# Performance work log

Measured on AMD Instinct MI355X. Metric: run time of the kernel, lower is better.

## Reference

```python
import jax, jax.numpy as jnp
import numpy as np

N_HEAD = 16
NEG_INF = -1e30  # finite mask value, safe for softmax/grad


def setup_inputs() -> dict:
    key = jax.random.key(0)
    k1, k2, k3 = jax.random.split(key, 3)
    B, T, C = 4, 2049, 1024
    x = jax.random.normal(k1, (B, T, C), dtype=jnp.float32)
    W_attn = jax.random.normal(k2, (C, 3 * C), dtype=jnp.float32) * (1.0 / np.sqrt(C))
    W_proj = jax.random.normal(k3, (C, C), dtype=jnp.float32) * (1.0 / np.sqrt(C))
    return {"x": x, "W_attn": W_attn, "W_proj": W_proj}


def reference(x, W_attn, W_proj):
    B, T, C = x.shape
    H = N_HEAD
    D = C // H
    qkv = x @ W_attn                                  # (B, T, 3C)
    q, k, v = jnp.split(qkv, 3, axis=-1)
    q = q.reshape(B, T, H, D).transpose(0, 2, 1, 3)   # (B, H, T, D)
    k = k.reshape(B, T, H, D).transpose(0, 2, 1, 3)
    v = v.reshape(B, T, H, D).transpose(0, 2, 1, 3)
    # hybrid mask: causal tril, but state token (row 0) attends to ALL positions
    mask = jnp.tril(jnp.ones((T, T), dtype=bool))
    mask = mask.at[0, :].set(True)
    scale = 1.0 / np.sqrt(D)
    scores = jnp.einsum('bhtd,bhsd->bhts', q, k) * scale
    scores = jnp.where(mask[None, None, :, :], scores, NEG_INF)
    att = jax.nn.softmax(scores, axis=-1)
    y = jnp.einsum('bhts,bhsd->bhtd', att, v)         # (B, H, T, D)
    y = y.transpose(0, 2, 1, 3).reshape(B, T, C)
    return y @ W_proj
```

## Files before the change

### kernel.cpp

```cpp
#include <hip/hip_runtime.h>

typedef __attribute__((ext_vector_type(8))) __bf16 bf16x8;
typedef __attribute__((ext_vector_type(4))) __bf16 bf16x4;
typedef __attribute__((ext_vector_type(4))) float f32x4;

#define GLDS(g, l) __builtin_amdgcn_global_load_lds( \
    (__attribute__((address_space(1))) void*)(void*)(g), \
    (__attribute__((address_space(3))) void*)(void*)(l), 16, 0, 0)

constexpr int T_REAL = 2049;
constexpr int Tp     = 2112;
constexpr int Mreal  = 8196;
constexpr int Mp     = 8448;
constexpr int GK     = 1024;

constexpr float QSCALE = 0.125f * 1.4426950408889634f;

__global__ __launch_bounds__(256) void cvt_x(const float* __restrict__ x,
                                             __bf16* __restrict__ xb) {
    size_t i = ((size_t)blockIdx.x * 256 + threadIdx.x) * 4;
    float4 v = make_float4(0.f, 0.f, 0.f, 0.f);
    if (i < (size_t)Mreal * GK) v = *(const float4*)(x + i);
    bf16x4 o;
    o.x = (__bf16)v.x; o.y = (__bf16)v.y; o.z = (__bf16)v.z; o.w = (__bf16)v.w;
    *(bf16x4*)(xb + i) = o;
}

__global__ __launch_bounds__(256) void transpose_w(const float* __restrict__ W,
                                                   __bf16* __restrict__ Wt,
                                                   int K, int N) {
    __shared__ float tile[64][65];
    const int n0 = blockIdx.x * 64, k0 = blockIdx.y * 64;
    const int tx = threadIdx.x & 63, ty = threadIdx.x >> 6;
#pragma unroll
    for (int j = 0; j < 16; j++) {
        int rk = ty + j * 4;
        tile[rk][tx] = W[(size_t)(k0 + rk) * N + n0 + tx];
    }
    __syncthreads();
#pragma unroll
    for (int j = 0; j < 16; j++) {
        int rn = ty + j * 4;
        Wt[(size_t)(n0 + rn) * K + k0 + tx] = (__bf16)tile[tx][rn];
    }
}

__global__ __launch_bounds__(256) void transpose_v(const __bf16* __restrict__ v,
                                                   __bf16* __restrict__ vT) {
    __shared__ __bf16 tl[64][72];
    const int bh = blockIdx.y, t0 = blockIdx.x * 64;
    const int tid = threadIdx.x;
    const __bf16* src = v + ((size_t)bh * Tp + t0) * 64;
    {
        const int r = tid >> 3, c = (tid & 7) * 8;
        *(bf16x8*)&tl[r][c]      = *(const bf16x8*)(src + r * 64 + c);
        *(bf16x8*)&tl[r + 32][c] = *(const bf16x8*)(src + (r + 32) * 64 + c);
    }
    __syncthreads();
    __bf16* dst = vT + (size_t)bh * 64 * Tp + t0;
    {
        const int d = tid >> 3, tc = (tid & 7) * 8;
        bf16x8 a, b;
#pragma unroll
        for (int i = 0; i < 8; i++) {
            a[i] = tl[tc + i][d];
            b[i] = tl[tc + i][d + 32];
        }
        *(bf16x8*)(dst + (size_t)d * Tp + tc)        = a;
        *(bf16x8*)(dst + (size_t)(d + 32) * Tp + tc) = b;
    }
}

__global__ __launch_bounds__(512)
void gemm256(const __bf16* __restrict__ A, const __bf16* __restrict__ Bt,
             __bf16* __restrict__ qout, __bf16* __restrict__ kout,
             __bf16* __restrict__ vout) {
    __shared__ __align__(16) __bf16 As[2][16384];
    __shared__ __align__(16) __bf16 Bs[2][16384];

    const int tid = threadIdx.x, lane = tid & 63, w = tid >> 6;
    const int wr = w >> 2, wc = w & 3;
    const int quad = lane >> 4, l15 = lane & 15, l7 = l15 & 7;
    const int m0 = blockIdx.y * 256, n0 = blockIdx.x * 256;

    const int sr = tid >> 3;
    const int sc = ((tid & 7) ^ (sr & 7)) * 8;
    const __bf16* ag = A  + (size_t)(m0 + sr) * GK + sc;
    const __bf16* bg = Bt + (size_t)(n0 + sr) * GK + sc;
    const int ldst = tid * 8;

#define STG_A(T, h) do { const __bf16* s_ = ag + (size_t)(h) * 128 * GK + (T) * 64; \
    GLDS(s_, &As[(T) & 1][(h) * 8192 + ldst]); \
    GLDS(s_ + (size_t)64 * GK, &As[(T) & 1][(h) * 8192 + 4096 + ldst]); } while (0)
#define STG_B(T, h) do { const __bf16* s_ = bg + (size_t)(h) * 128 * GK + (T) * 64; \
    GLDS(s_, &Bs[(T) & 1][(h) * 8192 + ldst]); \
    GLDS(s_ + (size_t)64 * GK, &Bs[(T) & 1][(h) * 8192 + 4096 + ldst]); } while (0)

    f32x4 acc[8][4] = {};
    bf16x8 a[8], b0[4], b1[4];

    STG_A(0, 0); STG_B(0, 1); STG_A(0, 1); STG_B(0, 0); STG_A(1, 0); STG_B(1, 1);
    asm volatile("s_waitcnt vmcnt(4)" ::: "memory");
    __builtin_amdgcn_s_barrier();

    constexpr int NT = GK / 64;

#pragma unroll 1
    for (int T = 0; T < NT; ++T) {
        const int p = T & 1;

#pragma unroll
        for (int f = 0; f < 4; ++f) {
            const int R = f * 32 + wr * 16 + l15;
            a[f * 2 + 0] = *(const bf16x8*)&As[p][R * 64 + ((quad ^ l7) * 8)];
            a[f * 2 + 1] = *(const bf16x8*)&As[p][R * 64 + (((4 + quad) ^ l7) * 8)];
        }
#pragma unroll
        for (int n = 0; n < 2; ++n) {
            const int R = n * 64 + wc * 16 + l15;
            b0[n * 2 + 0] = *(const bf16x8*)&Bs[p][R * 64 + ((quad ^ l7) * 8)];
            b0[n * 2 + 1] = *(const bf16x8*)&Bs[p][R * 64 + (((4 + quad) ^ l7) * 8)];
        }
        if (T + 1 < NT) { STG_A(T + 1, 1); STG_B(T + 1, 0); }
        __builtin_amdgcn_s_barrier();
        asm volatile("s_waitcnt lgkmcnt(0)" ::: "memory");
        __builtin_amdgcn_sched_barrier(0);
        __builtin_amdgcn_s_setprio(1);
#pragma unroll
        for (int f = 0; f < 4; ++f)
#pragma unroll
            for (int n = 0; n < 2; ++n) {
                acc[f][n] = __builtin_amdgcn_mfma_f32_16x16x32_bf16(a[f*2+0], b0[n*2+0], acc[f][n], 0, 0, 0);
                acc[f][n] = __builtin_amdgcn_mfma_f32_16x16x32_bf16(a[f*2+1], b0[n*2+1], acc[f][n], 0, 0, 0);
            }
        __builtin_amdgcn_s_setprio(0);
        __builtin_amdgcn_s_barrier();

#pragma unroll
        for (int n = 0; n < 2; ++n) {
            const int R = 128 + n * 64 + wc * 16 + l15;
            b1[n * 2 + 0] = *(const bf16x8*)&Bs[p][R * 64 + ((quad ^ l7) * 8)];
            b1[n * 2 + 1] = *(const bf16x8*)&Bs[p][R * 64 + (((4 + quad) ^ l7) * 8)];
        }
        __builtin_amdgcn_s_barrier();
        asm volatile("s_waitcnt lgkmcnt(0)" ::: "memory");
        __builtin_amdgcn_sched_barrier(0);
        __builtin_amdgcn_s_setprio(1);
#pragma unroll
        for (int f = 0; f < 4; ++f)
#pragma unroll
            for (int n = 0; n < 2; ++n) {
                acc[f][2+n] = __builtin_amdgcn_mfma_f32_16x16x32_bf16(a[f*2+0], b1[n*2+0], acc[f][2+n], 0, 0, 0);
                acc[f][2+n] = __builtin_amdgcn_mfma_f32_16x16x32_bf16(a[f*2+1], b1[n*2+1], acc[f][2+n], 0, 0, 0);
            }
        __builtin_amdgcn_s_setprio(0);
        __builtin_amdgcn_s_barrier();

#pragma unroll
        for (int f = 0; f < 4; ++f) {
            const int R = 128 + f * 32 + wr * 16 + l15;
            a[f * 2 + 0] = *(const bf16x8*)&As[p][R * 64 + ((quad ^ l7) * 8)];
            a[f * 2 + 1] = *(const bf16x8*)&As[p][R * 64 + (((4 + quad) ^ l7) * 8)];
        }
        if (T + 2 < NT) STG_A(T + 2, 0);
        __builtin_amdgcn_s_barrier();
        asm volatile("s_waitcnt lgkmcnt(0)" ::: "memory");
        __builtin_amdgcn_sched_barrier(0);
        __builtin_amdgcn_s_setprio(1);
#pragma unroll
        for (int f = 0; f < 4; ++f)
#pragma unroll
            for (int n = 0; n < 2; ++n) {
                acc[4+f][2+n] = __builtin_amdgcn_mfma_f32_16x16x32_bf16(a[f*2+0], b1[n*2+0], acc[4+f][2+n], 0, 0, 0);
                acc[4+f][2+n] = __builtin_amdgcn_mfma_f32_16x16x32_bf16(a[f*2+1], b1[n*2+1], acc[4+f][2+n], 0, 0, 0);
            }
        __builtin_amdgcn_s_setprio(0);
        __builtin_amdgcn_s_barrier();

        if (T + 2 < NT) STG_B(T + 2, 1);
        __builtin_amdgcn_s_barrier();
        asm volatile("s_waitcnt lgkmcnt(0)" ::: "memory");
        __builtin_amdgcn_sched_barrier(0);
        __builtin_amdgcn_s_setprio(1);
#pragma unroll
        for (int f = 0; f < 4; ++f)
#pragma unroll
            for (int n = 0; n < 2; ++n) {
                acc[4+f][n] = __builtin_amdgcn_mfma_f32_16x16x32_bf16(a[f*2+0], b0[n*2+0], acc[4+f][n], 0, 0, 0);
                acc[4+f][n] = __builtin_amdgcn_mfma_f32_16x16x32_bf16(a[f*2+1], b0[n*2+1], acc[4+f][n], 0, 0, 0);
            }
        __builtin_amdgcn_s_setprio(0);
        if (T < NT - 2) { asm volatile("s_waitcnt vmcnt(4)" ::: "memory"); }
        else            { asm volatile("s_waitcnt vmcnt(0)" ::: "memory"); }
        __builtin_amdgcn_s_barrier();
    }
#undef STG_A
#undef STG_B

    const int which = n0 >> 10;
    __bf16* op = (which == 0) ? qout : (which == 1) ? kout : vout;
    const float scl = (which == 0) ? QSCALE : 1.0f;
    __bf16* ep = &As[0][0];
    const int rr = tid >> 4, cc = tid & 15;
#pragma unroll
    for (int f = 0; f < 8; ++f) {
        __syncthreads();
#pragma unroll
        for (int n = 0; n < 4; ++n) {
            const int col = (n & 1) * 64 + wc * 16 + (n >> 1) * 128 + l15;
#pragma unroll
            for (int r = 0; r < 4; ++r)
                ep[(wr * 16 + quad * 4 + r) * 264 + col] = (__bf16)(acc[f][n][r] * scl);
        }
        __syncthreads();
        const int m = m0 + (f & 3) * 32 + (f >> 2) * 128 + rr;
        if (m < Mreal) {
            const int b = m / T_REAL;
            const int t = m - b * T_REAL;
#pragma unroll
            for (int g = 0; g < 2; ++g) {
                const int c8 = (cc + g * 16) * 8;
                bf16x8 vv = *(const bf16x8*)&ep[rr * 264 + c8];
                const int gc = n0 + c8;
                const int h = (gc >> 6) & 15;
                *(bf16x8*)&op[((size_t)(b * 16 + h) * Tp + t) * 64 + (gc & 63)] = vv;
            }
        }
    }
}

template <int EPI>
__global__ __launch_bounds__(256)
void gemm128(const __bf16* __restrict__ A, const __bf16* __restrict__ Bt,
             float* __restrict__ outp,
             __bf16* __restrict__ qout, __bf16* __restrict__ kout,
             __bf16* __restrict__ vout) {
    __shared__ __bf16 As[128 * 64];
    __shared__ __bf16 Bs[128 * 64];

    const int tid = threadIdx.x, lane = tid & 63, w = tid >> 6;
    const int wr = w >> 1, wc = w & 1;
    const int quad = lane >> 4, l15 = lane & 15, l7 = l15 & 7;
    const int m0 = blockIdx.y * 128, n0 = blockIdx.x * 128;

    const int row0 = w * 32 + (lane >> 3);
    const int gc8 = ((lane & 7) ^ ((lane >> 3) & 7)) * 8;
    const __bf16* agp = A + (size_t)(m0 + row0) * GK + gc8;
    const __bf16* bgp = Bt + (size_t)(n0 + row0) * GK + gc8;
    __bf16* lap = &As[(w * 256 + lane) * 8];
    __bf16* lbp = &Bs[(w * 256 + lane) * 8];

    f32x4 acc[4][4] = {};

    for (int k0 = 0; k0 < GK; k0 += 64) {
#pragma unroll
        for (int s = 0; s < 4; s++) {
            GLDS(agp + (size_t)s * 8 * GK + k0, lap + s * 512);
            GLDS(bgp + (size_t)s * 8 * GK + k0, lbp + s * 512);
        }
        __syncthreads();
#pragma unroll
        for (int kk = 0; kk < 2; kk++) {
            bf16x8 fa[4], fb[4];
#pragma unroll
            for (int i = 0; i < 4; i++)
                fa[i] = *(const bf16x8*)&As[(wr * 64 + i * 16 + l15) * 64 + (((kk * 4 + quad) ^ l7) * 8)];
#pragma unroll
            for (int j = 0; j < 4; j++)
                fb[j] = *(const bf16x8*)&Bs[(wc * 64 + j * 16 + l15) * 64 + (((kk * 4 + quad) ^ l7) * 8)];
#pragma unroll
            for (int i = 0; i < 4; i++)
#pragma unroll
                for (int j = 0; j < 4; j++)
                    acc[i][j] = __builtin_amdgcn_mfma_f32_16x16x32_bf16(fa[i], fb[j], acc[i][j], 0, 0, 0);
        }
        __syncthreads();
    }

    if constexpr (EPI == 0) {
        const int which = n0 >> 10;
        const int h = ((n0 + wc * 64) >> 6) & 15;
        __bf16* op = (which == 0) ? qout : (which == 1) ? kout : vout;
        const float scl = (which == 0) ? QSCALE : 1.0f;
        __bf16* wls = &As[w * 2048];
#pragma unroll
        for (int p = 0; p < 2; p++) {
            if (p) __syncthreads();
#pragma unroll
            for (int i2 = 0; i2 < 2; i2++)
#pragma unroll
                for (int j = 0; j < 4; j++)
#pragma unroll
                    for (int r = 0; r < 4; r++) {
                        const int lrow = i2 * 16 + quad * 4 + r;
                        const int cX = (j * 2 + (l15 >> 3)) ^ (lrow & 7);
                        wls[lrow * 64 + cX * 8 + (l15 & 7)] =
                            (__bf16)(acc[p * 2 + i2][j][r] * scl);
                    }
            __syncthreads();
#pragma unroll
            for (int it = 0; it < 4; it++) {
                const int lrow = (lane >> 3) + it * 8;
                bf16x8 vv = *(const bf16x8*)&wls[lrow * 64 + (((lane & 7) ^ (lrow & 7)) * 8)];
                const int m = m0 + wr * 64 + p * 32 + lrow;
                if (m < Mreal) {
                    const int b = m / T_REAL;
                    const int t = m - b * T_REAL;
                    *(bf16x8*)&op[(((size_t)(b * 16 + h)) * Tp + t) * 64 + (lane & 7) * 8] = vv;
                }
            }
        }
    } else {
        float* wlf = (float*)&As[0] + w * 1024;
#pragma unroll
        for (int p = 0; p < 4; p++) {
            if (p) __syncthreads();
#pragma unroll
            for (int j = 0; j < 4; j++)
#pragma unroll
                for (int r = 0; r < 4; r++) {
                    const int lrow = quad * 4 + r;
                    const int cX = (j * 4 + (l15 >> 2)) ^ (lrow & 7);
                    wlf[lrow * 64 + cX * 4 + (l15 & 3)] = acc[p][j][r];
                }
            __syncthreads();
#pragma unroll
            for (int it = 0; it < 4; it++) {
                const int lrow = lane >> 2;
                const int c = (lane & 3) + it * 4;
                f32x4 vv = *(const f32x4*)&wlf[lrow * 64 + ((c ^ (lrow & 7)) * 4)];
                const int m = m0 + wr * 64 + p * 16 + lrow;
                if (m < Mreal)
                    *(f32x4*)&outp[(size_t)m * 1024 + n0 + wc * 64 + c * 4] = vv;
            }
        }
    }
}

__global__ __launch_bounds__(512, 8)
void attn(const __bf16* __restrict__ q, const __bf16* __restrict__ kk,
          const __bf16* __restrict__ vT, __bf16* __restrict__ y) {
    __shared__ __bf16 Ks[2][64 * 64];
    __shared__ __bf16 Vs[2][64 * 64];
    __shared__ __bf16 Pq[8][16 * 32];

    static const int QA[17] = {0,31,29,27,25,23,21,19,17,15,13,11,9,7,5,3,1};
    static const int QB[17] = {32,30,28,26,24,22,20,18,16,14,12,10,8,6,4,2,-1};

    const int tid = threadIdx.x, lane = tid & 63, w = tid >> 6;
    const int quad = lane >> 4, l15 = lane & 15;
    const int l7 = l15 & 7;
    const int z = blockIdx.x;
    const int slot = z >> 6;
    const int zz = z & 63;
    const int bh = (zz & 7) * 8 + (zz >> 3);

    const int qtA = QA[slot];
    const int qt = (w < 4) ? qtA : QB[slot];
    const bool active = qt >= 0;
    const int qts = active ? qt : 0;
    const int q0 = qts * 64;
    const int qg = q0 + (w & 3) * 16 + l15;
    const int myNt = (qts == 0) ? 32 : qts;
    const int ntmaxB = (qtA == 0) ? 32 : qtA;

    const __bf16* kgb = kk + (size_t)bh * Tp * 64;
    const __bf16* vgb = vT + (size_t)bh * 64 * Tp;
    const int b = bh >> 4, h = bh & 15;

    const int r0 = tid >> 3;
    const int s0 = ((tid & 7) ^ (r0 & 7)) * 8;
    const int koff = r0 * 64 + s0;
    const int voff = r0 * Tp + s0;

    const int pswz = (((l15 >> 1) & 3) << 1) ^ ((l15 >> 3) << 2);

    bf16x8 qa0, qa1;
    {
        const __bf16* qp = q + ((size_t)bh * Tp + qg) * 64 + quad * 8;
        qa0 = *(const bf16x8*)qp;
        qa1 = *(const bf16x8*)(qp + 32);
    }

    f32x4 o[4] = {};
    float mrow = -3e38f, lrow = 0.f;

    GLDS(kgb + koff, &Ks[0][tid * 8]);
    GLDS(vgb + voff, &Vs[0][tid * 8]);

    int cur = 0;
    for (int nt = 0; nt <= ntmaxB; ++nt) {
        __syncthreads();
        if (nt < ntmaxB) {
            GLDS(kgb + (size_t)(nt + 1) * 4096 + koff, &Ks[cur ^ 1][tid * 8]);
            GLDS(vgb + (size_t)(nt + 1) * 64 + voff, &Vs[cur ^ 1][tid * 8]);
        }
        if (active && nt <= myNt) {
            const int kv0 = nt * 64;

            f32x4 st[4];
#pragma unroll
            for (int j = 0; j < 4; j++) {
                const __bf16* krow = &Ks[cur][(j * 16 + l15) * 64];
                bf16x8 klo = *(const bf16x8*)(krow + ((quad ^ l7) * 8));
                bf16x8 khi = *(const bf16x8*)(krow + (((quad + 4) ^ l7) * 8));
                f32x4 zzv = {0.f, 0.f, 0.f, 0.f};
                zzv = __builtin_amdgcn_mfma_f32_16x16x32_bf16(klo, qa0, zzv, 0, 0, 0);
                st[j] = __builtin_amdgcn_mfma_f32_16x16x32_bf16(khi, qa1, zzv, 0, 0, 0);
            }

            if (nt >= qts) {
#pragma unroll
                for (int j = 0; j < 4; j++)
#pragma unroll
                    for (int r = 0; r < 4; r++) {
                        const int kvg = kv0 + j * 16 + quad * 4 + r;
                        const bool valid = (kvg <= qg) || (qg == 0 && kvg < T_REAL);
                        st[j][r] = valid ? st[j][r] : -1e30f;
                    }
            }

            float mx = -3e38f;
#pragma unroll
            for (int j = 0; j < 4; j++)
#pragma unroll
                for (int r = 0; r < 4; r++) mx = fmaxf(mx, st[j][r]);
            mx = fmaxf(mx, __shfl_xor(mx, 16));
            mx = fmaxf(mx, __shfl_xor(mx, 32));
            if (!__all(mx - mrow <= 8.0f)) {
                const float mn = fmaxf(mrow, mx);
                const float alpha = __builtin_amdgcn_exp2f(mrow - mn);
                mrow = mn;
                lrow *= alpha;
#pragma unroll
                for (int nf = 0; nf < 4; nf++)
#pragma unroll
                    for (int r = 0; r < 4; r++) o[nf][r] *= alpha;
            }

            float rs = 0.f;
            bf16x4 pk[4];
#pragma unroll
            for (int j = 0; j < 4; j++) {
                float p0 = __builtin_amdgcn_exp2f(st[j][0] - mrow);
                float p1 = __builtin_amdgcn_exp2f(st[j][1] - mrow);
                float p2 = __builtin_amdgcn_exp2f(st[j][2] - mrow);
                float p3 = __builtin_amdgcn_exp2f(st[j][3] - mrow);
                rs += (p0 + p1) + (p2 + p3);
                pk[j].x = (__bf16)p0; pk[j].y = (__bf16)p1;
                pk[j].z = (__bf16)p2; pk[j].w = (__bf16)p3;
            }
            rs += __shfl_xor(rs, 16);
            rs += __shfl_xor(rs, 32);
            lrow += rs;

#pragma unroll
            for (int h2 = 0; h2 < 2; ++h2) {
                *(bf16x4*)&Pq[w][l15 * 32 + (((0 + quad) ^ pswz) * 4)] = pk[2 * h2];
                *(bf16x4*)&Pq[w][l15 * 32 + (((4 + quad) ^ pswz) * 4)] = pk[2 * h2 + 1];
                bf16x8 pb = *(const bf16x8*)&Pq[w][l15 * 32 + (((quad * 2) ^ pswz) * 4)];
#pragma unroll
                for (int nf = 0; nf < 4; nf++) {
                    bf16x8 va = *(const bf16x8*)&Vs[cur][(nf * 16 + l15) * 64 + (((h2 * 4 + quad) ^ l7) * 8)];
                    o[nf] = __builtin_amdgcn_mfma_f32_16x16x32_bf16(va, pb, o[nf], 0, 0, 0);
                }
            }
        }
        cur ^= 1;
    }

    if (active && qg < T_REAL) {
        const float inv = 1.0f / lrow;
        __bf16* yp = y + ((size_t)(b * T_REAL + qg)) * 1024 + h * 64 + quad * 4;
#pragma unroll
        for (int nf = 0; nf < 4; nf++) {
            bf16x4 pko;
            pko.x = (__bf16)(o[nf][0] * inv);
            pko.y = (__bf16)(o[nf][1] * inv);
            pko.z = (__bf16)(o[nf][2] * inv);
            pko.w = (__bf16)(o[nf][3] * inv);
            *(bf16x4*)(yp + nf * 16) = pko;
        }
    }
}

extern "C" void kernel_launch(void* const* d_in, const int* in_sizes, int n_in,
                              void* d_out, int out_size, void* d_ws, size_t ws_size,
                              hipStream_t stream) {
    const float* x  = (const float*)d_in[0];
    const float* Wa = (const float*)d_in[1];
    const float* Wp = (const float*)d_in[2];
    float* out = (float*)d_out;

    char* ws = (char*)d_ws;
    constexpr size_t SZ_XB  = (size_t)Mp * GK * 2;
    constexpr size_t SZ_WAT = (size_t)3072 * GK * 2;
    constexpr size_t SZ_WPT = (size_t)1024 * GK * 2;
    constexpr size_t SZ_QK  = (size_t)64 * Tp * 64 * 2;
    __bf16* xb   = (__bf16*)(ws);
    __bf16* WaT  = (__bf16*)(ws + SZ_XB);
    __bf16* WpT  = (__bf16*)(ws + SZ_XB + SZ_WAT);
    __bf16* qb   = (__bf16*)(ws + SZ_XB + SZ_WAT + SZ_WPT);
    __bf16* kb   = (__bf16*)(ws + SZ_XB + SZ_WAT + SZ_WPT + SZ_QK);
    __bf16* vTb  = (__bf16*)(ws + SZ_XB + SZ_WAT + SZ_WPT + 2 * SZ_QK);
    __bf16* shrd = (__bf16*)(ws + SZ_XB + SZ_WAT + SZ_WPT + 3 * SZ_QK);
    __bf16* vpre = shrd;
    __bf16* yb   = shrd;

    cvt_x<<<(Mp * GK) / 1024, 256, 0, stream>>>(x, xb);
    transpose_w<<<dim3(48, 16), 256, 0, stream>>>(Wa, WaT, 1024, 3072);
    transpose_w<<<dim3(16, 16), 256, 0, stream>>>(Wp, WpT, 1024, 1024);

    gemm256<<<dim3(12, 33), 512, 0, stream>>>(xb, WaT, qb, kb, vpre);
    transpose_v<<<dim3(33, 64), 256, 0, stream>>>(vpre, vTb);
    attn<<<1088, 512, 0, stream>>>(qb, kb, vTb, yb);
    gemm128<1><<<dim3(8, 65), 256, 0, stream>>>(yb, WpT, out, nullptr, nullptr, nullptr);
}
```

Baseline: 291.2 us.

## Switch attention to 32x32x16 MFMA with register-only P via permlane32 swap

Rewrites the attention inner loop to use 32x32x16 bf16 MFMA, with each wave owning 32 query rows and blocks shrunk to 256 threads. The P matrix is packed with v_cvt_pk_bf16_f32 and rearranged across lanes with v_permlane32_swap, which removes the LDS round trip through the Pq buffer. The aim is fewer MFMA issues, fewer shuffles and less LDS traffic per tile. In exchange, register pressure rises and each block has fewer waves to hide load latency.

```diff
diff --git a/kernel.cpp b/kernel.cpp
--- a/kernel.cpp
+++ b/kernel.cpp
@@ -3,6 +3,7 @@
 typedef __attribute__((ext_vector_type(8))) __bf16 bf16x8;
 typedef __attribute__((ext_vector_type(4))) __bf16 bf16x4;
 typedef __attribute__((ext_vector_type(4))) float f32x4;
+typedef __attribute__((ext_vector_type(16))) float f32x16;
 
 #define GLDS(g, l) __builtin_amdgcn_global_load_lds( \
     (__attribute__((address_space(1))) void*)(void*)(g), \
@@ -337,30 +338,26 @@
     }
 }
 
-__global__ __launch_bounds__(512, 8)
+__global__ __launch_bounds__(256, 4)
 void attn(const __bf16* __restrict__ q, const __bf16* __restrict__ kk,
           const __bf16* __restrict__ vT, __bf16* __restrict__ y) {
     __shared__ __bf16 Ks[2][64 * 64];
     __shared__ __bf16 Vs[2][64 * 64];
-    __shared__ __bf16 Pq[8][16 * 32];
 
     static const int QA[17] = {0,31,29,27,25,23,21,19,17,15,13,11,9,7,5,3,1};
     static const int QB[17] = {32,30,28,26,24,22,20,18,16,14,12,10,8,6,4,2,-1};
 
     const int tid = threadIdx.x, lane = tid & 63, w = tid >> 6;
-    const int quad = lane >> 4, l15 = lane & 15;
-    const int l7 = l15 & 7;
+    const int l31 = lane & 31, hi = lane >> 5, l7 = l31 & 7;
     const int z = blockIdx.x;
-    const int slot = z >> 6;
-    const int zz = z & 63;
+    const int slot = z >> 6, zz = z & 63;
     const int bh = (zz & 7) * 8 + (zz >> 3);
 
     const int qtA = QA[slot];
-    const int qt = (w < 4) ? qtA : QB[slot];
+    const int qt = (w < 2) ? qtA : QB[slot];
     const bool active = qt >= 0;
     const int qts = active ? qt : 0;
-    const int q0 = qts * 64;
-    const int qg = q0 + (w & 3) * 16 + l15;
+    const int qg = qts * 64 + (w & 1) * 32 + l31;
     const int myNt = (qts == 0) ? 32 : qts;
     const int ntmaxB = (qtA == 0) ? 32 : qtA;
 
@@ -368,64 +365,67 @@
     const __bf16* vgb = vT + (size_t)bh * 64 * Tp;
     const int b = bh >> 4, h = bh & 15;
 
-    const int r0 = tid >> 3;
-    const int s0 = ((tid & 7) ^ (r0 & 7)) * 8;
-    const int koff = r0 * 64 + s0;
-    const int voff = r0 * Tp + s0;
-
-    const int pswz = (((l15 >> 1) & 3) << 1) ^ ((l15 >> 3) << 2);
-
-    bf16x8 qa0, qa1;
+    const int sr = lane >> 3;
+    const int scol = ((lane & 7) ^ sr) * 8;
+    const int rk = w * 16 + sr;
+    const int ldk = w * 1024 + lane * 8;
+
+    bf16x8 qa[4];
     {
-        const __bf16* qp = q + ((size_t)bh * Tp + qg) * 64 + quad * 8;
-        qa0 = *(const bf16x8*)qp;
-        qa1 = *(const bf16x8*)(qp + 32);
-    }
-
-    f32x4 o[4] = {};
+        const __bf16* qp = q + ((size_t)bh * Tp + qg) * 64 + hi * 8;
+#pragma unroll
+        for (int s = 0; s < 4; ++s) qa[s] = *(const bf16x8*)(qp + s * 16);
+    }
+
+    f32x16 o0 = {}, o1 = {};
     float mrow = -3e38f, lrow = 0.f;
 
-    GLDS(kgb + koff, &Ks[0][tid * 8]);
-    GLDS(vgb + voff, &Vs[0][tid * 8]);
+    GLDS(kgb + rk * 64 + scol,               &Ks[0][ldk]);
+    GLDS(kgb + (rk + 8) * 64 + scol,         &Ks[0][ldk + 512]);
+    GLDS(vgb + (size_t)rk * Tp + scol,       &Vs[0][ldk]);
+    GLDS(vgb + (size_t)(rk + 8) * Tp + scol, &Vs[0][ldk + 512]);
 
     int cur = 0;
     for (int nt = 0; nt <= ntmaxB; ++nt) {
         __syncthreads();
         if (nt < ntmaxB) {
-            GLDS(kgb + (size_t)(nt + 1) * 4096 + koff, &Ks[cur ^ 1][tid * 8]);
-            GLDS(vgb + (size_t)(nt + 1) * 64 + voff, &Vs[cur ^ 1][tid * 8]);
+            const size_t ko = (size_t)(nt + 1) * 4096;
+            const size_t vo = (size_t)(nt + 1) * 64;
+            GLDS(kgb + ko + rk * 64 + scol,               &Ks[cur ^ 1][ldk]);
+            GLDS(kgb + ko + (rk + 8) * 64 + scol,         &Ks[cur ^ 1][ldk + 512]);
+            GLDS(vgb + vo + (size_t)rk * Tp + scol,       &Vs[cur ^ 1][ldk]);
+            GLDS(vgb + vo + (size_t)(rk + 8) * Tp + scol, &Vs[cur ^ 1][ldk + 512]);
         }
         if (active && nt <= myNt) {
             const int kv0 = nt * 64;
 
-            f32x4 st[4];
-#pragma unroll
-            for (int j = 0; j < 4; j++) {
-                const __bf16* krow = &Ks[cur][(j * 16 + l15) * 64];
-                bf16x8 klo = *(const bf16x8*)(krow + ((quad ^ l7) * 8));
-                bf16x8 khi = *(const bf16x8*)(krow + (((quad + 4) ^ l7) * 8));
-                f32x4 zzv = {0.f, 0.f, 0.f, 0.f};
-                zzv = __builtin_amdgcn_mfma_f32_16x16x32_bf16(klo, qa0, zzv, 0, 0, 0);
-                st[j] = __builtin_amdgcn_mfma_f32_16x16x32_bf16(khi, qa1, zzv, 0, 0, 0);
+            f32x16 s0 = {}, s1 = {};
+#pragma unroll
+            for (int sl = 0; sl < 4; ++sl) {
+                const int ch = ((sl * 2 + hi) ^ l7) * 8;
+                bf16x8 k0 = *(const bf16x8*)&Ks[cur][l31 * 64 + ch];
+                bf16x8 k1 = *(const bf16x8*)&Ks[cur][(32 + l31) * 64 + ch];
+                s0 = __builtin_amdgcn_mfma_f32_32x32x16_bf16(k0, qa[sl], s0, 0, 0, 0);
+                s1 = __builtin_amdgcn_mfma_f32_32x32x16_bf16(k1, qa[sl], s1, 0, 0, 0);
             }
 
             if (nt >= qts) {
 #pragma unroll
-                for (int j = 0; j < 4; j++)
-#pragma unroll
-                    for (int r = 0; r < 4; r++) {
-                        const int kvg = kv0 + j * 16 + quad * 4 + r;
-                        const bool valid = (kvg <= qg) || (qg == 0 && kvg < T_REAL);
-                        st[j][r] = valid ? st[j][r] : -1e30f;
-                    }
+                for (int t = 0; t < 16; ++t) {
+                    const int kvg = kv0 + (t & 3) + 8 * (t >> 2) + 4 * hi;
+                    const bool v0 = (kvg <= qg) || (qg == 0 && kvg < T_REAL);
+                    const bool v1 = (kvg + 32 <= qg) || (qg == 0 && kvg + 32 < T_REAL);
+                    s0[t] = v0 ? s0[t] : -1e30f;
+                    s1[t] = v1 ? s1[t] : -1e30f;
+                }
             }
 
             float mx = -3e38f;
 #pragma unroll
-            for (int j = 0; j < 4; j++)
-#pragma unroll
-                for (int r = 0; r < 4; r++) mx = fmaxf(mx, st[j][r]);
-            mx = fmaxf(mx, __shfl_xor(mx, 16));
+            for (int t = 0; t < 16; ++t) {
+                mx = fmaxf(mx, s0[t]);
+                mx = fmaxf(mx, s1[t]);
+            }
             mx = fmaxf(mx, __shfl_xor(mx, 32));
             if (!__all(mx - mrow <= 8.0f)) {
                 const float mn = fmaxf(mrow, mx);
@@ -433,37 +433,38 @@
                 mrow = mn;
                 lrow *= alpha;
 #pragma unroll
-                for (int nf = 0; nf < 4; nf++)
-#pragma unroll
-                    for (int r = 0; r < 4; r++) o[nf][r] *= alpha;
+                for (int t = 0; t < 16; ++t) { o0[t] *= alpha; o1[t] *= alpha; }
             }
 
             float rs = 0.f;
-            bf16x4 pk[4];
-#pragma unroll
-            for (int j = 0; j < 4; j++) {
-                float p0 = __builtin_amdgcn_exp2f(st[j][0] - mrow);
-                float p1 = __builtin_amdgcn_exp2f(st[j][1] - mrow);
-                float p2 = __builtin_amdgcn_exp2f(st[j][2] - mrow);
-                float p3 = __builtin_amdgcn_exp2f(st[j][3] - mrow);
-                rs += (p0 + p1) + (p2 + p3);
-                pk[j].x = (__bf16)p0; pk[j].y = (__bf16)p1;
-                pk[j].z = (__bf16)p2; pk[j].w = (__bf16)p3;
-            }
-            rs += __shfl_xor(rs, 16);
+#pragma unroll
+            for (int t = 0; t < 16; ++t) {
+                s0[t] = __builtin_amdgcn_exp2f(s0[t] - mrow);
+                s1[t] = __builtin_amdgcn_exp2f(s1[t] - mrow);
+                rs += s0[t] + s1[t];
+            }
             rs += __shfl_xor(rs, 32);
             lrow += rs;
 
 #pragma unroll
-            for (int h2 = 0; h2 < 2; ++h2) {
-                *(bf16x4*)&Pq[w][l15 * 32 + (((0 + quad) ^ pswz) * 4)] = pk[2 * h2];
-                *(bf16x4*)&Pq[w][l15 * 32 + (((4 + quad) ^ pswz) * 4)] = pk[2 * h2 + 1];
-                bf16x8 pb = *(const bf16x8*)&Pq[w][l15 * 32 + (((quad * 2) ^ pswz) * 4)];
-#pragma unroll
-                for (int nf = 0; nf < 4; nf++) {
-                    bf16x8 va = *(const bf16x8*)&Vs[cur][(nf * 16 + l15) * 64 + (((h2 * 4 + quad) ^ l7) * 8)];
-                    o[nf] = __builtin_amdgcn_mfma_f32_16x16x32_bf16(va, pb, o[nf], 0, 0, 0);
-                }
+            for (int m = 0; m < 4; ++m) {
+                const f32x16 sb = (m & 2) ? s1 : s0;
+                constexpr int SB8[4] = {0, 8, 0, 8};
+                const int s8 = SB8[m];
+                unsigned a01, a23, a45, a67;
+                asm("v_cvt_pk_bf16_f32 %0, %1, %2" : "=v"(a01) : "v"(sb[s8 + 0]), "v"(sb[s8 + 1]));
+                asm("v_cvt_pk_bf16_f32 %0, %1, %2" : "=v"(a23) : "v"(sb[s8 + 2]), "v"(sb[s8 + 3]));
+                asm("v_cvt_pk_bf16_f32 %0, %1, %2" : "=v"(a45) : "v"(sb[s8 + 4]), "v"(sb[s8 + 5]));
+                asm("v_cvt_pk_bf16_f32 %0, %1, %2" : "=v"(a67) : "v"(sb[s8 + 6]), "v"(sb[s8 + 7]));
+                asm("v_permlane32_swap_b32 %0, %1" : "+v"(a01), "+v"(a45));
+                asm("v_permlane32_swap_b32 %0, %1" : "+v"(a23), "+v"(a67));
+                union { unsigned u[4]; bf16x8 v; } pf;
+                pf.u[0] = a01; pf.u[1] = a23; pf.u[2] = a45; pf.u[3] = a67;
+                const int ch = ((m * 2 + hi) ^ l7) * 8;
+                bf16x8 v0 = *(const bf16x8*)&Vs[cur][l31 * 64 + ch];
+                bf16x8 v1 = *(const bf16x8*)&Vs[cur][(32 + l31) * 64 + ch];
+                o0 = __builtin_amdgcn_mfma_f32_32x32x16_bf16(v0, pf.v, o0, 0, 0, 0);
+                o1 = __builtin_amdgcn_mfma_f32_32x32x16_bf16(v1, pf.v, o1, 0, 0, 0);
             }
         }
         cur ^= 1;
@@ -471,15 +472,20 @@
 
     if (active && qg < T_REAL) {
         const float inv = 1.0f / lrow;
-        __bf16* yp = y + ((size_t)(b * T_REAL + qg)) * 1024 + h * 64 + quad * 4;
-#pragma unroll
-        for (int nf = 0; nf < 4; nf++) {
-            bf16x4 pko;
-            pko.x = (__bf16)(o[nf][0] * inv);
-            pko.y = (__bf16)(o[nf][1] * inv);
-            pko.z = (__bf16)(o[nf][2] * inv);
-            pko.w = (__bf16)(o[nf][3] * inv);
-            *(bf16x4*)(yp + nf * 16) = pko;
+        __bf16* yp = y + ((size_t)(b * T_REAL + qg)) * 1024 + h * 64 + hi * 4;
+#pragma unroll
+        for (int g = 0; g < 4; ++g) {
+            bf16x4 w0, w1;
+            w0.x = (__bf16)(o0[g * 4 + 0] * inv);
+            w0.y = (__bf16)(o0[g * 4 + 1] * inv);
+            w0.z = (__bf16)(o0[g * 4 + 2] * inv);
+            w0.w = (__bf16)(o0[g * 4 + 3] * inv);
+            w1.x = (__bf16)(o1[g * 4 + 0] * inv);
+            w1.y = (__bf16)(o1[g * 4 + 1] * inv);
+            w1.z = (__bf16)(o1[g * 4 + 2] * inv);
+            w1.w = (__bf16)(o1[g * 4 + 3] * inv);
+            *(bf16x4*)(yp + g * 8)      = w0;
+            *(bf16x4*)(yp + 32 + g * 8) = w1;
         }
     }
 }
@@ -513,6 +519,6 @@
 
     gemm256<<<dim3(12, 33), 512, 0, stream>>>(xb, WaT, qb, kb, vpre);
     transpose_v<<<dim3(33, 64), 256, 0, stream>>>(vpre, vTb);
-    attn<<<1088, 512, 0, stream>>>(qb, kb, vTb, yb);
+    attn<<<1088, 256, 0, stream>>>(qb, kb, vTb, yb);
     gemm128<1><<<dim3(8, 65), 256, 0, stream>>>(yb, WpT, out, nullptr, nullptr, nullptr);
 }
```

After: 277.1 us. 4.9% less time.
